# Performance work log

Measured on AMD Instinct MI355X. Metric: run time of the kernel, lower is better.

## Reference

```python
import jax, jax.numpy as jnp
import numpy as np

H = 4096
W = 4096
C = 3
OUT = 1024
MAX_MIP = 8  # matches init max_mip_level; mip chain is levels 0..MAX_MIP


def setup_inputs() -> dict:
    key = jax.random.key(0)
    k1, k2, k3 = jax.random.split(key, 3)
    data = jax.random.uniform(k1, (1, H, W, C), dtype=jnp.float32)
    texc = jax.random.uniform(k2, (1, OUT, OUT, 2), dtype=jnp.float32)
    # small UV derivatives -> per-pixel texel footprint of a few texels, so the
    # LOD spans several mip levels (exercises cross-level paged gathers)
    texc_deriv = jax.random.normal(k3, (1, OUT, OUT, 4), dtype=jnp.float32) * 2e-3
    return {"data": data, "texc": texc, "texc_deriv": texc_deriv}


def _avg_pool2(x):
    # 2x2 box-filter mipmap reduction, matching virtual_texture_mipmap_fwd
    b, h, w, c = x.shape
    return x.reshape(b, h // 2, 2, w // 2, 2, c).mean(axis=(2, 4))


def _bilinear_wrap(tex, texc):
    # tex: [1,h,w,c]; texc: [1,Ho,Wo,2] in [0,1); boundary_mode='wrap'
    h, w = tex.shape[1], tex.shape[2]
    x = texc[..., 0] * w - 0.5
    y = texc[..., 1] * h - 0.5
    x0f = jnp.floor(x)
    y0f = jnp.floor(y)
    fx = (x - x0f)[..., None]
    fy = (y - y0f)[..., None]
    x0 = x0f.astype(jnp.int32) % w
    y0 = y0f.astype(jnp.int32) % h
    x1 = (x0 + 1) % w
    y1 = (y0 + 1) % h
    t = tex[0]  # [h,w,c]
    top = t[y0, x0] * (1.0 - fx) + t[y0, x1] * fx
    bot = t[y1, x0] * (1.0 - fx) + t[y1, x1] * fx
    return top * (1.0 - fy) + bot * fy  # [1,Ho,Wo,c]


def _forward(data, texc, texc_deriv):
    # LOD from screen-space UV derivatives (nvdiffrast linear-mipmap-linear)
    dudx = texc_deriv[..., 0] * W
    dvdx = texc_deriv[..., 1] * H
    dudy = texc_deriv[..., 2] * W
    dvdy = texc_deriv[..., 3] * H
    rho2 = jnp.maximum(dudx * dudx + dvdx * dvdx, dudy * dudy + dvdy * dvdy)
    lod = 0.5 * jnp.log2(jnp.maximum(rho2, 1e-20))
    lod = jnp.clip(lod, 0.0, float(MAX_MIP))  # [1,Ho,Wo]

    # build mip pyramid (gradients flow back to base texture, matching
    # virtual_texture_mipmap_bwd accumulation)
    mips = [data]
    for _ in range(MAX_MIP):
        mips.append(_avg_pool2(mips[-1]))

    # trilinear: per-level weight w_l = clip(1 - |lod - l|, 0, 1)
    out = jnp.zeros(texc.shape[:-1] + (C,), dtype=data.dtype)
    for lvl in range(MAX_MIP + 1):
        w_l = jnp.clip(1.0 - jnp.abs(lod - float(lvl)), 0.0, 1.0)[..., None]
        out = out + w_l * _bilinear_wrap(mips[lvl], texc)
    return out


def reference(data, texc, texc_deriv):
    return _forward(data, texc, texc_deriv)
```

## Files before the change

kernel.cpp:

```cpp
#include <hip/hip_runtime.h>
#include <hip/hip_bf16.h>


#define OUT_N (1024 * 1024)

__device__ __forceinline__ unsigned mip_off_b(int lvl) {
    return (67108864u - (67108864u >> (2 * lvl - 2))) / 3u;
}
#define OFF2 16777216u
#define OFF3 20971520u
#define OFF4 22020096u
#define OFF5 22282240u
#define OFF6 22347776u

__device__ __forceinline__ unsigned pack10(float r, float g, float b) {
    unsigned ur = __float2uint_rn(r * 1023.0f);
    unsigned ug = __float2uint_rn(g * 1023.0f);
    unsigned ub = __float2uint_rn(b * 1023.0f);
    return ur | (ug << 10) | (ub << 20);
}

__device__ __forceinline__ void dec_acc(unsigned q, float w, float& r, float& g, float& b) {
    const float s = 1.0f / 1023.0f;
    r = fmaf((float)(q & 1023u) * s, w, r);
    g = fmaf((float)((q >> 10) & 1023u) * s, w, g);
    b = fmaf((float)((q >> 20) & 1023u) * s, w, b);
}

__device__ __forceinline__ float4 dec4(unsigned q) {
    const float s = 1.0f / 1023.0f;
    return float4{(float)(q & 1023u) * s, (float)((q >> 10) & 1023u) * s,
                  (float)((q >> 20) & 1023u) * s, 0.0f};
}

__device__ __forceinline__ float4 avg4(float4 a, float4 b, float4 c, float4 d) {
    return float4{(a.x + b.x + c.x + d.x) * 0.25f,
                  (a.y + b.y + c.y + d.y) * 0.25f,
                  (a.z + b.z + c.z + d.z) * 0.25f, 0.0f};
}

__device__ __forceinline__ void store_quad(char* p, float4 t00, float4 t01,
                                           float4 t10, float4 t11) {
    *(uint4*)p = make_uint4(pack10(t00.x, t00.y, t00.z), pack10(t01.x, t01.y, t01.z),
                            pack10(t10.x, t10.y, t10.z), pack10(t11.x, t11.y, t11.z));
}

__global__ __launch_bounds__(256, 4) void mip_fused(const float* __restrict__ data,
                                                    char* __restrict__ wsb) {
    __shared__ float4 s2[32][33];
    __shared__ float4 s3[16][17];
    __shared__ float4 s4[8][9];
    __shared__ float4 s5[4][5];

    const int t = threadIdx.x;
    const int bx = blockIdx.x & 31;
    const int by = blockIdx.x >> 5;

    {
        int qx = t & 15, qy = t >> 4;
        int r0 = (by << 7) + (qy << 3);
        int c0 = (bx << 7) + (qx << 3);
        const float* p0 = data + ((size_t)r0 * 4096 + c0) * 3;
        float4 t00 = {0, 0, 0, 0}, t01 = {0, 0, 0, 0};
        float4 t10 = {0, 0, 0, 0}, t11 = {0, 0, 0, 0};
#pragma unroll
        for (int i = 0; i < 8; ++i) {
            const float4* rp = (const float4*)(p0 + (size_t)i * (4096 * 3));
            float4 A = rp[0], Bv = rp[1], Cv = rp[2];
            float4 D = rp[3], E = rp[4], F = rp[5];
            float lx = A.x + A.w + Bv.z + Cv.y;
            float ly = A.y + Bv.x + Bv.w + Cv.z;
            float lz = A.z + Bv.y + Cv.x + Cv.w;
            float rx = D.x + D.w + E.z + F.y;
            float ry = D.y + E.x + E.w + F.z;
            float rz = D.z + E.y + F.x + F.w;
            if (i < 4) {
                t00.x += lx; t00.y += ly; t00.z += lz;
                t01.x += rx; t01.y += ry; t01.z += rz;
            } else {
                t10.x += lx; t10.y += ly; t10.z += lz;
                t11.x += rx; t11.y += ry; t11.z += rz;
            }
        }
        const float sc = 1.0f / 16.0f;
        t00.x *= sc; t00.y *= sc; t00.z *= sc;
        t01.x *= sc; t01.y *= sc; t01.z *= sc;
        t10.x *= sc; t10.y *= sc; t10.z *= sc;
        t11.x *= sc; t11.y *= sc; t11.z *= sc;
        s2[2 * qy][2 * qx] = t00;     s2[2 * qy][2 * qx + 1] = t01;
        s2[2 * qy + 1][2 * qx] = t10; s2[2 * qy + 1][2 * qx + 1] = t11;
        unsigned gq = ((by << 4) + qy) * 512u + (bx << 4) + qx;
        store_quad(wsb + OFF2 + ((size_t)gq << 4), t00, t01, t10, t11);
    }
    __syncthreads();

    if (t < 64) {
        int qx = t & 7, qy = t >> 3;
        int sy = qy << 2, sx = qx << 2;
        float4 t00 = avg4(s2[sy][sx], s2[sy][sx + 1], s2[sy + 1][sx], s2[sy + 1][sx + 1]);
        float4 t01 = avg4(s2[sy][sx + 2], s2[sy][sx + 3], s2[sy + 1][sx + 2], s2[sy + 1][sx + 3]);
        float4 t10 = avg4(s2[sy + 2][sx], s2[sy + 2][sx + 1], s2[sy + 3][sx], s2[sy + 3][sx + 1]);
        float4 t11 = avg4(s2[sy + 2][sx + 2], s2[sy + 2][sx + 3], s2[sy + 3][sx + 2], s2[sy + 3][sx + 3]);
        s3[2 * qy][2 * qx] = t00;     s3[2 * qy][2 * qx + 1] = t01;
        s3[2 * qy + 1][2 * qx] = t10; s3[2 * qy + 1][2 * qx + 1] = t11;
        unsigned gq = ((by << 3) + qy) * 256u + (bx << 3) + qx;
        store_quad(wsb + OFF3 + ((size_t)gq << 4), t00, t01, t10, t11);
    }
    __syncthreads();

    if (t < 16) {
        int qx = t & 3, qy = t >> 2;
        int sy = qy << 2, sx = qx << 2;
        float4 t00 = avg4(s3[sy][sx], s3[sy][sx + 1], s3[sy + 1][sx], s3[sy + 1][sx + 1]);
        float4 t01 = avg4(s3[sy][sx + 2], s3[sy][sx + 3], s3[sy + 1][sx + 2], s3[sy + 1][sx + 3]);
        float4 t10 = avg4(s3[sy + 2][sx], s3[sy + 2][sx + 1], s3[sy + 3][sx], s3[sy + 3][sx + 1]);
        float4 t11 = avg4(s3[sy + 2][sx + 2], s3[sy + 2][sx + 3], s3[sy + 3][sx + 2], s3[sy + 3][sx + 3]);
        s4[2 * qy][2 * qx] = t00;     s4[2 * qy][2 * qx + 1] = t01;
        s4[2 * qy + 1][2 * qx] = t10; s4[2 * qy + 1][2 * qx + 1] = t11;
        unsigned gq = ((by << 2) + qy) * 128u + (bx << 2) + qx;
        store_quad(wsb + OFF4 + ((size_t)gq << 4), t00, t01, t10, t11);
    }
    __syncthreads();

    if (t < 4) {
        int qx = t & 1, qy = t >> 1;
        int sy = qy << 2, sx = qx << 2;
        float4 t00 = avg4(s4[sy][sx], s4[sy][sx + 1], s4[sy + 1][sx], s4[sy + 1][sx + 1]);
        float4 t01 = avg4(s4[sy][sx + 2], s4[sy][sx + 3], s4[sy + 1][sx + 2], s4[sy + 1][sx + 3]);
        float4 t10 = avg4(s4[sy + 2][sx], s4[sy + 2][sx + 1], s4[sy + 3][sx], s4[sy + 3][sx + 1]);
        float4 t11 = avg4(s4[sy + 2][sx + 2], s4[sy + 2][sx + 3], s4[sy + 3][sx + 2], s4[sy + 3][sx + 3]);
        s5[2 * qy][2 * qx] = t00;     s5[2 * qy][2 * qx + 1] = t01;
        s5[2 * qy + 1][2 * qx] = t10; s5[2 * qy + 1][2 * qx + 1] = t11;
        unsigned gq = ((by << 1) + qy) * 64u + (bx << 1) + qx;
        store_quad(wsb + OFF5 + ((size_t)gq << 4), t00, t01, t10, t11);
    }
    __syncthreads();

    if (t == 0) {
        float4 t00 = avg4(s5[0][0], s5[0][1], s5[1][0], s5[1][1]);
        float4 t01 = avg4(s5[0][2], s5[0][3], s5[1][2], s5[1][3]);
        float4 t10 = avg4(s5[2][0], s5[2][1], s5[3][0], s5[3][1]);
        float4 t11 = avg4(s5[2][2], s5[2][3], s5[3][2], s5[3][3]);
        unsigned gq = (unsigned)by * 32u + (unsigned)bx;
        store_quad(wsb + OFF6 + ((size_t)gq << 4), t00, t01, t10, t11);
    }
}

__device__ __forceinline__ void tap_off(int lvl, float u, float v,
                                        unsigned& o00, unsigned& o01,
                                        unsigned& o10, unsigned& o11,
                                        float& fx, float& fy) {
    int size = 4096 >> lvl;
    float fs = (float)size;
    float x = fmaf(u, fs, -0.5f);
    float y = fmaf(v, fs, -0.5f);
    float x0f = floorf(x);
    float y0f = floorf(y);
    fx = x - x0f;
    fy = y - y0f;
    int m = size - 1;
    int x0 = ((int)x0f) & m;
    int y0 = ((int)y0f) & m;
    int x1 = (x0 + 1) & m;
    int y1 = (y0 + 1) & m;
    int hs = size >> 1;
    unsigned r0 = (unsigned)((y0 >> 1) * hs);
    unsigned r1 = (unsigned)((y1 >> 1) * hs);
    unsigned c0 = (unsigned)(x0 >> 1), c1 = (unsigned)(x1 >> 1);
    unsigned sy0 = (unsigned)((y0 & 1) << 3), sy1 = (unsigned)((y1 & 1) << 3);
    unsigned sx0 = (unsigned)((x0 & 1) << 2), sx1 = (unsigned)((x1 & 1) << 2);
    o00 = ((r0 + c0) << 4) + sy0 + sx0;
    o01 = ((r0 + c1) << 4) + sy0 + sx1;
    o10 = ((r1 + c0) << 4) + sy1 + sx0;
    o11 = ((r1 + c1) << 4) + sy1 + sx1;
}

__device__ __forceinline__ void sample_packed(const char* __restrict__ wsb, int lvl,
                                              float u, float v, float wgt,
                                              float& r, float& g, float& b) {
    unsigned o00, o01, o10, o11;
    float fx, fy;
    tap_off(lvl, u, v, o00, o01, o10, o11, fx, fy);
    const char* B = wsb + mip_off_b(lvl);
    unsigned q00 = *(const unsigned*)(B + o00);
    unsigned q01 = *(const unsigned*)(B + o01);
    unsigned q10 = *(const unsigned*)(B + o10);
    unsigned q11 = *(const unsigned*)(B + o11);
    dec_acc(q00, (1.0f - fx) * (1.0f - fy) * wgt, r, g, b);
    dec_acc(q01, fx * (1.0f - fy) * wgt, r, g, b);
    dec_acc(q10, (1.0f - fx) * fy * wgt, r, g, b);
    dec_acc(q11, fx * fy * wgt, r, g, b);
}

__device__ void sample_fine(const float* __restrict__ data, int lvl,
                            float u, float v, float wgt,
                            float& r, float& g, float& b) {
    int size = 4096 >> lvl;
    float fs = (float)size;
    float x = u * fs - 0.5f;
    float y = v * fs - 0.5f;
    float x0f = floorf(x);
    float y0f = floorf(y);
    float fx = x - x0f;
    float fy = y - y0f;
    int m = size - 1;
    int x0 = ((int)x0f) & m;
    int y0 = ((int)y0f) & m;
    int x1 = (x0 + 1) & m;
    int y1 = (y0 + 1) & m;
    int k = 1 << lvl;
    float inv = wgt / (float)(k * k);
    float ww[2][2] = {{(1.0f - fx) * (1.0f - fy) * inv, fx * (1.0f - fy) * inv},
                      {(1.0f - fx) * fy * inv, fx * fy * inv}};
    int xs[2] = {x0 << lvl, x1 << lvl};
    int ys[2] = {y0 << lvl, y1 << lvl};
    for (int ty = 0; ty < 2; ++ty)
        for (int tx = 0; tx < 2; ++tx) {
            float tr = 0.0f, tg = 0.0f, tb = 0.0f;
            for (int dy = 0; dy < k; ++dy)
                for (int dx = 0; dx < k; ++dx) {
                    const float* p = data + ((size_t)(ys[ty] + dy) * 4096 + xs[tx] + dx) * 3;
                    tr += p[0]; tg += p[1]; tb += p[2];
                }
            r = fmaf(tr, ww[ty][tx], r);
            g = fmaf(tg, ww[ty][tx], g);
            b = fmaf(tb, ww[ty][tx], b);
        }
}

__device__ float4 read_l6(const char* __restrict__ wsb, int xx, int yy) {
    size_t a = OFF6 + ((((yy >> 1) * 32) + (xx >> 1)) << 4) + ((yy & 1) << 3) + ((xx & 1) << 2);
    return dec4(*(const unsigned*)(wsb + a));
}

__device__ void sample_coarse(const char* __restrict__ wsb, int lvl,
                              float u, float v, float wgt,
                              float& r, float& g, float& b) {
    int size = 4096 >> lvl;
    float fs = (float)size;
    float x = u * fs - 0.5f;
    float y = v * fs - 0.5f;
    float x0f = floorf(x);
    float y0f = floorf(y);
    float fx = x - x0f;
    float fy = y - y0f;
    int m = size - 1;
    int x0 = ((int)x0f) & m;
    int y0 = ((int)y0f) & m;
    int x1 = (x0 + 1) & m;
    int y1 = (y0 + 1) & m;
    int s = lvl - 6;
    int k = 1 << s;
    float inv = wgt / (float)(k * k);
    float ww[2][2] = {{(1.0f - fx) * (1.0f - fy) * inv, fx * (1.0f - fy) * inv},
                      {(1.0f - fx) * fy * inv, fx * fy * inv}};
    int xs[2] = {x0 << s, x1 << s};
    int ys[2] = {y0 << s, y1 << s};
    for (int ty = 0; ty < 2; ++ty)
        for (int tx = 0; tx < 2; ++tx) {
            float tr = 0.0f, tg = 0.0f, tb = 0.0f;
            for (int dy = 0; dy < k; ++dy)
                for (int dx = 0; dx < k; ++dx) {
                    float4 c = read_l6(wsb, xs[tx] + dx, ys[ty] + dy);
                    tr += c.x; tg += c.y; tb += c.z;
                }
            r = fmaf(tr, ww[ty][tx], r);
            g = fmaf(tg, ww[ty][tx], g);
            b = fmaf(tb, ww[ty][tx], b);
        }
}

__device__ __forceinline__ void sample_any(const float* __restrict__ data,
                                           const char* __restrict__ wsb, int lvl,
                                           float u, float v, float wgt,
                                           float& r, float& g, float& b) {
    if (lvl >= 2) {
        if (lvl <= 6) sample_packed(wsb, lvl, u, v, wgt, r, g, b);
        else sample_coarse(wsb, lvl, u, v, wgt, r, g, b);
    } else {
        sample_fine(data, lvl, u, v, wgt, r, g, b);
    }
}

__global__ __launch_bounds__(256, 4) void vt_sample(const float* __restrict__ data,
                                                    const char* __restrict__ wsb,
                                                    const float* __restrict__ texc,
                                                    const float* __restrict__ deriv,
                                                    float* __restrict__ out) {
    int p = blockIdx.x * 256 + threadIdx.x;

    float2 uv = ((const float2*)texc)[p];
    float4 dv = ((const float4*)deriv)[p];
    float dudx = dv.x * 4096.0f;
    float dvdx = dv.y * 4096.0f;
    float dudy = dv.z * 4096.0f;
    float dvdy = dv.w * 4096.0f;
    float rho2 = fmaxf(fmaf(dudx, dudx, dvdx * dvdx), fmaf(dudy, dudy, dvdy * dvdy));
    float lod = 0.5f * __log2f(fmaxf(rho2, 1e-20f));
    lod = fminf(fmaxf(lod, 0.0f), 8.0f);

    int l0 = (int)lod;
    float f = lod - (float)l0;
    int l1 = (l0 < 8) ? (l0 + 1) : 8;

    float r = 0.0f, g = 0.0f, b = 0.0f;

    if (__builtin_expect((unsigned)(l0 - 2) <= 3u, 1)) {
        unsigned a00, a01, a10, a11, b00, b01, b10, b11;
        float fx0, fy0, fx1, fy1;
        const char* B0 = wsb + mip_off_b(l0);
        const char* B1 = wsb + mip_off_b(l1);
        tap_off(l0, uv.x, uv.y, a00, a01, a10, a11, fx0, fy0);
        tap_off(l1, uv.x, uv.y, b00, b01, b10, b11, fx1, fy1);
        unsigned q0 = *(const unsigned*)(B0 + a00);
        unsigned q1 = *(const unsigned*)(B0 + a01);
        unsigned q2 = *(const unsigned*)(B0 + a10);
        unsigned q3 = *(const unsigned*)(B0 + a11);
        unsigned q4 = *(const unsigned*)(B1 + b00);
        unsigned q5 = *(const unsigned*)(B1 + b01);
        unsigned q6 = *(const unsigned*)(B1 + b10);
        unsigned q7 = *(const unsigned*)(B1 + b11);
        float w0 = 1.0f - f;
        dec_acc(q0, (1.0f - fx0) * (1.0f - fy0) * w0, r, g, b);
        dec_acc(q1, fx0 * (1.0f - fy0) * w0, r, g, b);
        dec_acc(q2, (1.0f - fx0) * fy0 * w0, r, g, b);
        dec_acc(q3, fx0 * fy0 * w0, r, g, b);
        dec_acc(q4, (1.0f - fx1) * (1.0f - fy1) * f, r, g, b);
        dec_acc(q5, fx1 * (1.0f - fy1) * f, r, g, b);
        dec_acc(q6, (1.0f - fx1) * fy1 * f, r, g, b);
        dec_acc(q7, fx1 * fy1 * f, r, g, b);
    } else {
        sample_any(data, wsb, l0, uv.x, uv.y, 1.0f - f, r, g, b);
        sample_any(data, wsb, l1, uv.x, uv.y, f, r, g, b);
    }

    float* o = out + (size_t)p * 3;
    o[0] = r;
    o[1] = g;
    o[2] = b;
}

extern "C" void kernel_launch(void* const* d_in, const int* in_sizes, int n_in,
                              void* d_out, int out_size, void* d_ws, size_t ws_size,
                              hipStream_t stream) {
    const float* data  = (const float*)d_in[0];
    const float* texc  = (const float*)d_in[1];
    const float* deriv = (const float*)d_in[2];
    float* out = (float*)d_out;
    char* wsb  = (char*)d_ws;

    mip_fused<<<1024, 256, 0, stream>>>(data, wsb);
    vt_sample<<<OUT_N / 256, 256, 0, stream>>>(data, wsb, texc, deriv, out);
}
```

Before: 369.1 us.

## Stage mip source tiles via global_load_lds into shared memory with smaller blocks

The mip-building kernel now moves each 64x64 texel tile straight from global memory into LDS with async global_load_lds. Threads then reduce from LDS, where before each thread issued strided float4 row loads itself. Blocks drop from 128x128 to 64x64 tiles, so the grid grows fourfold. The top level is written as individual packed words into the shared quad layout. Launch-bound occupancy hints are relaxed on both kernels. The aim is more memory-level parallelism and better coalescing on the 200MB input read, at the cost of 53KB of LDS per block, which limits occupancy.

```diff
diff --git a/kernel.cpp b/kernel.cpp
--- a/kernel.cpp
+++ b/kernel.cpp
@@ -45,104 +45,93 @@
                             pack10(t10.x, t10.y, t10.z), pack10(t11.x, t11.y, t11.z));
 }
 
-__global__ __launch_bounds__(256, 4) void mip_fused(const float* __restrict__ data,
-                                                    char* __restrict__ wsb) {
-    __shared__ float4 s2[32][33];
-    __shared__ float4 s3[16][17];
-    __shared__ float4 s4[8][9];
-    __shared__ float4 s5[4][5];
+#define POOL_BYTES (49152 + 4352)
+
+__global__ __launch_bounds__(256) void mip_fused(const float* __restrict__ data,
+                                                 char* __restrict__ wsb) {
+    __shared__ float4 pool4[POOL_BYTES / 16];
+    char* pool = (char*)pool4;
+    float4(*s2)[17] = (float4(*)[17])(pool + 49152);
+    float4(*s3)[9]  = (float4(*)[9])(pool + 0);
+    float4(*s4)[5]  = (float4(*)[5])(pool + 2048);
+    float4(*s5)[3]  = (float4(*)[3])(pool + 4096);
 
     const int t = threadIdx.x;
-    const int bx = blockIdx.x & 31;
-    const int by = blockIdx.x >> 5;
+    const int bx = blockIdx.x & 63;
+    const int by = blockIdx.x >> 6;
 
     {
-        int qx = t & 15, qy = t >> 4;
-        int r0 = (by << 7) + (qy << 3);
-        int c0 = (bx << 7) + (qx << 3);
-        const float* p0 = data + ((size_t)r0 * 4096 + c0) * 3;
-        float4 t00 = {0, 0, 0, 0}, t01 = {0, 0, 0, 0};
-        float4 t10 = {0, 0, 0, 0}, t11 = {0, 0, 0, 0};
+        const char* src = (const char*)data + (size_t)by * 64 * 49152 + (size_t)bx * 768;
 #pragma unroll
-        for (int i = 0; i < 8; ++i) {
-            const float4* rp = (const float4*)(p0 + (size_t)i * (4096 * 3));
+        for (int j = 0; j < 12; ++j) {
+            int f = t + j * 256;
+            int row = f / 48;
+            int col = f - row * 48;
+            const char* g = src + (size_t)row * 49152 + (size_t)col * 16;
+            __builtin_amdgcn_global_load_lds(
+                (const __attribute__((address_space(1))) unsigned int*)g,
+                (__attribute__((address_space(3))) unsigned int*)(pool + (size_t)f * 16),
+                16, 0, 0);
+        }
+    }
+    __syncthreads();
+
+    {
+        int tx = t & 15, ty = t >> 4;
+        float rr = 0.0f, gg = 0.0f, bb = 0.0f;
+#pragma unroll
+        for (int i = 0; i < 4; ++i) {
+            const float4* rp = (const float4*)(pool + (size_t)(4 * ty + i) * 768 + (size_t)tx * 48);
             float4 A = rp[0], Bv = rp[1], Cv = rp[2];
-            float4 D = rp[3], E = rp[4], F = rp[5];
-            float lx = A.x + A.w + Bv.z + Cv.y;
-            float ly = A.y + Bv.x + Bv.w + Cv.z;
-            float lz = A.z + Bv.y + Cv.x + Cv.w;
-            float rx = D.x + D.w + E.z + F.y;
-            float ry = D.y + E.x + E.w + F.z;
-            float rz = D.z + E.y + F.x + F.w;
-            if (i < 4) {
-                t00.x += lx; t00.y += ly; t00.z += lz;
-                t01.x += rx; t01.y += ry; t01.z += rz;
-            } else {
-                t10.x += lx; t10.y += ly; t10.z += lz;
-                t11.x += rx; t11.y += ry; t11.z += rz;
-            }
+            rr += A.x + A.w + Bv.z + Cv.y;
+            gg += A.y + Bv.x + Bv.w + Cv.z;
+            bb += A.z + Bv.y + Cv.x + Cv.w;
         }
         const float sc = 1.0f / 16.0f;
-        t00.x *= sc; t00.y *= sc; t00.z *= sc;
-        t01.x *= sc; t01.y *= sc; t01.z *= sc;
-        t10.x *= sc; t10.y *= sc; t10.z *= sc;
-        t11.x *= sc; t11.y *= sc; t11.z *= sc;
-        s2[2 * qy][2 * qx] = t00;     s2[2 * qy][2 * qx + 1] = t01;
-        s2[2 * qy + 1][2 * qx] = t10; s2[2 * qy + 1][2 * qx + 1] = t11;
-        unsigned gq = ((by << 4) + qy) * 512u + (bx << 4) + qx;
-        store_quad(wsb + OFF2 + ((size_t)gq << 4), t00, t01, t10, t11);
+        float4 tex = {rr * sc, gg * sc, bb * sc, 0.0f};
+        __syncthreads();
+        s2[ty][tx] = tex;
     }
     __syncthreads();
 
     if (t < 64) {
         int qx = t & 7, qy = t >> 3;
-        int sy = qy << 2, sx = qx << 2;
-        float4 t00 = avg4(s2[sy][sx], s2[sy][sx + 1], s2[sy + 1][sx], s2[sy + 1][sx + 1]);
-        float4 t01 = avg4(s2[sy][sx + 2], s2[sy][sx + 3], s2[sy + 1][sx + 2], s2[sy + 1][sx + 3]);
-        float4 t10 = avg4(s2[sy + 2][sx], s2[sy + 2][sx + 1], s2[sy + 3][sx], s2[sy + 3][sx + 1]);
-        float4 t11 = avg4(s2[sy + 2][sx + 2], s2[sy + 2][sx + 3], s2[sy + 3][sx + 2], s2[sy + 3][sx + 3]);
-        s3[2 * qy][2 * qx] = t00;     s3[2 * qy][2 * qx + 1] = t01;
-        s3[2 * qy + 1][2 * qx] = t10; s3[2 * qy + 1][2 * qx + 1] = t11;
-        unsigned gq = ((by << 3) + qy) * 256u + (bx << 3) + qx;
-        store_quad(wsb + OFF3 + ((size_t)gq << 4), t00, t01, t10, t11);
+        float4 t00 = s2[2 * qy][2 * qx],     t01 = s2[2 * qy][2 * qx + 1];
+        float4 t10 = s2[2 * qy + 1][2 * qx], t11 = s2[2 * qy + 1][2 * qx + 1];
+        unsigned gq = ((by << 3) + qy) * 512u + (bx << 3) + qx;
+        store_quad(wsb + OFF2 + ((size_t)gq << 4), t00, t01, t10, t11);
+        s3[qy][qx] = avg4(t00, t01, t10, t11);
     }
     __syncthreads();
 
     if (t < 16) {
         int qx = t & 3, qy = t >> 2;
-        int sy = qy << 2, sx = qx << 2;
-        float4 t00 = avg4(s3[sy][sx], s3[sy][sx + 1], s3[sy + 1][sx], s3[sy + 1][sx + 1]);
-        float4 t01 = avg4(s3[sy][sx + 2], s3[sy][sx + 3], s3[sy + 1][sx + 2], s3[sy + 1][sx + 3]);
-        float4 t10 = avg4(s3[sy + 2][sx], s3[sy + 2][sx + 1], s3[sy + 3][sx], s3[sy + 3][sx + 1]);
-        float4 t11 = avg4(s3[sy + 2][sx + 2], s3[sy + 2][sx + 3], s3[sy + 3][sx + 2], s3[sy + 3][sx + 3]);
-        s4[2 * qy][2 * qx] = t00;     s4[2 * qy][2 * qx + 1] = t01;
-        s4[2 * qy + 1][2 * qx] = t10; s4[2 * qy + 1][2 * qx + 1] = t11;
-        unsigned gq = ((by << 2) + qy) * 128u + (bx << 2) + qx;
-        store_quad(wsb + OFF4 + ((size_t)gq << 4), t00, t01, t10, t11);
+        float4 t00 = s3[2 * qy][2 * qx],     t01 = s3[2 * qy][2 * qx + 1];
+        float4 t10 = s3[2 * qy + 1][2 * qx], t11 = s3[2 * qy + 1][2 * qx + 1];
+        unsigned gq = ((by << 2) + qy) * 256u + (bx << 2) + qx;
+        store_quad(wsb + OFF3 + ((size_t)gq << 4), t00, t01, t10, t11);
+        s4[qy][qx] = avg4(t00, t01, t10, t11);
     }
     __syncthreads();
 
     if (t < 4) {
         int qx = t & 1, qy = t >> 1;
-        int sy = qy << 2, sx = qx << 2;
-        float4 t00 = avg4(s4[sy][sx], s4[sy][sx + 1], s4[sy + 1][sx], s4[sy + 1][sx + 1]);
-        float4 t01 = avg4(s4[sy][sx + 2], s4[sy][sx + 3], s4[sy + 1][sx + 2], s4[sy + 1][sx + 3]);
-        float4 t10 = avg4(s4[sy + 2][sx], s4[sy + 2][sx + 1], s4[sy + 3][sx], s4[sy + 3][sx + 1]);
-        float4 t11 = avg4(s4[sy + 2][sx + 2], s4[sy + 2][sx + 3], s4[sy + 3][sx + 2], s4[sy + 3][sx + 3]);
-        s5[2 * qy][2 * qx] = t00;     s5[2 * qy][2 * qx + 1] = t01;
-        s5[2 * qy + 1][2 * qx] = t10; s5[2 * qy + 1][2 * qx + 1] = t11;
-        unsigned gq = ((by << 1) + qy) * 64u + (bx << 1) + qx;
+        float4 t00 = s4[2 * qy][2 * qx],     t01 = s4[2 * qy][2 * qx + 1];
+        float4 t10 = s4[2 * qy + 1][2 * qx], t11 = s4[2 * qy + 1][2 * qx + 1];
+        unsigned gq = ((by << 1) + qy) * 128u + (bx << 1) + qx;
+        store_quad(wsb + OFF4 + ((size_t)gq << 4), t00, t01, t10, t11);
+        s5[qy][qx] = avg4(t00, t01, t10, t11);
+    }
+    __syncthreads();
+
+    if (t == 0) {
+        float4 t00 = s5[0][0], t01 = s5[0][1], t10 = s5[1][0], t11 = s5[1][1];
+        unsigned gq = (unsigned)by * 64u + (unsigned)bx;
         store_quad(wsb + OFF5 + ((size_t)gq << 4), t00, t01, t10, t11);
-    }
-    __syncthreads();
-
-    if (t == 0) {
-        float4 t00 = avg4(s5[0][0], s5[0][1], s5[1][0], s5[1][1]);
-        float4 t01 = avg4(s5[0][2], s5[0][3], s5[1][2], s5[1][3]);
-        float4 t10 = avg4(s5[2][0], s5[2][1], s5[3][0], s5[3][1]);
-        float4 t11 = avg4(s5[2][2], s5[2][3], s5[3][2], s5[3][3]);
-        unsigned gq = (unsigned)by * 32u + (unsigned)bx;
-        store_quad(wsb + OFF6 + ((size_t)gq << 4), t00, t01, t10, t11);
+        float4 l6 = avg4(t00, t01, t10, t11);
+        size_t a6 = OFF6 + ((((by >> 1) * 32) + (bx >> 1)) << 4) +
+                    ((by & 1) << 3) + ((bx & 1) << 2);
+        *(unsigned*)(wsb + a6) = pack10(l6.x, l6.y, l6.z);
     }
 }
 
@@ -282,11 +271,11 @@
     }
 }
 
-__global__ __launch_bounds__(256, 4) void vt_sample(const float* __restrict__ data,
-                                                    const char* __restrict__ wsb,
-                                                    const float* __restrict__ texc,
-                                                    const float* __restrict__ deriv,
-                                                    float* __restrict__ out) {
+__global__ __launch_bounds__(256) void vt_sample(const float* __restrict__ data,
+                                                 const char* __restrict__ wsb,
+                                                 const float* __restrict__ texc,
+                                                 const float* __restrict__ deriv,
+                                                 float* __restrict__ out) {
     int p = blockIdx.x * 256 + threadIdx.x;
 
     float2 uv = ((const float2*)texc)[p];
@@ -349,6 +338,6 @@
     float* out = (float*)d_out;
     char* wsb  = (char*)d_ws;
 
-    mip_fused<<<1024, 256, 0, stream>>>(data, wsb);
+    mip_fused<<<4096, 256, 0, stream>>>(data, wsb);
     vt_sample<<<OUT_N / 256, 256, 0, stream>>>(data, wsb, texc, deriv, out);
 }
```

After: 327.0 us (median of 2 runs). 11.4% less time.
